# Kernel optimization log

Measured on AMD Instinct MI355X. Metric: run time of the kernel, lower is better.

## Reference

```python
import jax, jax.numpy as jnp
import numpy as np
from jax import lax

EPOCHS = 3
KS = [2, 3, 4, 5]
GRID_D = 5           # sqrt(25): covariance viewed as 5x5 grid of flat indices
M_OUT = 18           # AttentionManifold output SPD size

def _sub_idx(d, k):
    # flat indices of k*k x k*k principal submatrices (stride-1 windows), per SubManifold
    starts = np.arange(0, d - k + 1)
    ir, ic = np.meshgrid(starts, starts, indexing='ij')
    base = (ir * d + ic).reshape(-1)                       # [num_windows]
    a, b = np.meshgrid(np.arange(k), np.arange(k), indexing='ij')
    rel = (a * d + b).reshape(-1)                          # [k*k]
    return base[:, None] + rel[None, :]                    # [num_windows, k*k]

SUB_IDX = [_sub_idx(GRID_D, k) for k in KS]
IN_DIMS = [k * k for k in KS]                              # [4, 9, 16, 25]
IU = np.triu_indices(M_OUT)                                # 171 tangent features
TRI_COEF = np.where(IU[0] == IU[1], 1.0, np.sqrt(2.0)).astype(np.float32)

def _sym_fn(x, fn):
    w, u = jnp.linalg.eigh(x)
    return jnp.einsum('...ik,...k,...jk->...ij', u, fn(w), u)

def spd_log(x, floor=1e-9):
    # matrix log of SPD matrix (== torch.svd-based log for PD input)
    return _sym_fn(x, lambda w: jnp.log(jnp.clip(w, floor)))

def spd_exp(x):
    return _sym_fn(x, jnp.exp)

def spd_rect(x, eps=1e-4):
    # SPDRectified (ReEig): clamp eigenvalues from below
    return _sym_fn(x, lambda w: jnp.clip(w, eps))

def bimap(X, W):
    # SPDTransform: W^T X W, W: [d_in, d_out]
    return jnp.einsum('ia,...ij,jb->...ab', W, X, W)

def diag_jitter(x):
    # deterministic analogue of the random diagonal jitter in SubmanifoldAttention.tensor_log
    n = x.shape[-1]
    return x + jnp.diag((1e-4 / n) * (1.0 + jnp.arange(n, dtype=x.dtype)))

def signal2spd(x):
    # x: [B, C, T] -> trace-normalized covariance [B, C, C]
    x = x - x.mean(-1, keepdims=True)
    cov = jnp.einsum('bct,bdt->bcd', x, x) / (x.shape[-1] - 1)
    tra = jnp.trace(cov, axis1=-2, axis2=-1)[:, None, None]
    cov = cov / tra
    return cov + 1e-5 * jnp.eye(cov.shape[-1], dtype=cov.dtype)

def spd_attention(Q, K, V, jitter):
    # log-maps computed once per element; pairwise log-Euclidean distance via Frobenius identity
    if jitter:
        Q, K, V = diag_jitter(Q), diag_jitter(K), diag_jitter(V)
    logQ, logK = spd_log(Q), spd_log(K)
    qn = jnp.sum(logQ * logQ, (-2, -1))                    # [B, m]
    kn = jnp.sum(logK * logK, (-2, -1))
    cross = jnp.einsum('bixy,bjxy->bij', logK, logQ)
    # E[b,i,j] = ||logQ_j - logK_i||_F^2  (sum of singular values of D D^T)
    E = jnp.maximum(kn[:, :, None] + qn[:, None, :] - 2.0 * cross, 0.0)
    score = 1.0 / (1.0 + jnp.log1p(E))
    P = jnp.swapaxes(jax.nn.softmax(score, axis=-2), -1, -2)  # softmax over i, then permute
    B, m, sz, _ = V.shape
    logV = spd_log(V).reshape(B, m, sz * sz)
    out_log = (P @ logV).reshape(B, m, sz, sz)             # log-Euclidean weighted mean
    out_log = 0.5 * (out_log + jnp.swapaxes(out_log, -1, -2))
    return spd_exp(out_log)

def _bn(y, g, b, m, v):
    inv = g / jnp.sqrt(v + 1e-5)
    return (y - m[None, :, None, None]) * inv[None, :, None, None] + b[None, :, None, None]

def _forward(x, c1w, c1b, bn1g, bn1b, bn1m, bn1v, c2w, c2b, bn2g, bn2b, bn2m, bn2v,
             sq0, sq1, sq2, sq3, sk0, sk1, sk2, sk3, sv0, sv1, sv2, sv3,
             mq, mk, mv, lw, lb):
    dn = ('NCHW', 'OIHW', 'NCHW')
    y = lax.conv_general_dilated(x, c1w, (1, 1), 'VALID', dimension_numbers=dn) + c1b[None, :, None, None]
    y = _bn(y, bn1g, bn1b, bn1m, bn1v)
    y = lax.conv_general_dilated(y, c2w, (1, 1), [(0, 0), (6, 6)], dimension_numbers=dn) + c2b[None, :, None, None]
    y = _bn(y, bn2g, bn2b, bn2m, bn2v)
    sig = y[:, :, 0, :]                                    # squeeze -> [B, 25, T+1]
    T = sig.shape[-1]
    base = T // EPOCHS
    lens = [base + (1 if i < T - base * EPOCHS else 0) for i in range(EPOCHS)]
    covs, off = [], 0
    for Lp in lens:
        covs.append(signal2spd(sig[..., off:off + Lp])); off += Lp
    covs = jnp.stack(covs, axis=1)                         # [B, 3, 25, 25]
    sqs = [sq0, sq1, sq2, sq3]; sks = [sk0, sk1, sk2, sk3]; svs = [sv0, sv1, sv2, sv3]
    branch = []
    for t in range(EPOCHS):
        xb = covs[:, t]                                    # [B, 25, 25]
        Qs, Ks, Vs = [], [], []
        for gi, idx in enumerate(SUB_IDX):
            sub = xb[:, idx[:, :, None], idx[:, None, :]]  # [B, nw, k*k, k*k]
            Qs.append(bimap(sub, sqs[gi]))
            Ks.append(bimap(sub, sks[gi]))
            Vs.append(bimap(sub, svs[gi]))
        att = spd_attention(jnp.concatenate(Qs, 1), jnp.concatenate(Ks, 1),
                            jnp.concatenate(Vs, 1), jitter=True)   # [B, 30, 25, 25]
        branch.append(spd_rect(att[:, -1]))                # keep_only_last
    xm = jnp.stack(branch, axis=1)                         # [B, 3, 25, 25]
    att2 = spd_attention(bimap(xm, mq), bimap(xm, mk), bimap(xm, mv), jitter=False)
    Lg = spd_log(spd_rect(att2))                           # [B, 3, 18, 18]
    feat = (Lg[..., IU[0], IU[1]] * jnp.asarray(TRI_COEF)).reshape(xm.shape[0], -1)
    return feat @ lw.T + lb                                # [B, 4]

def setup_inputs():
    B, T = 256, 1000
    key = jax.random.key(0)
    ks = jax.random.split(key, 40)
    def ortho(k, din, dout):
        a = jax.random.normal(k, (max(din, dout), min(din, dout)), dtype=jnp.float32)
        q, _ = jnp.linalg.qr(a)
        return q if din >= dout else q.T
    inp = {
        'x': jax.random.normal(ks[0], (B, 1, 22, T), dtype=jnp.float32),
        'c1w': 0.1 * jax.random.normal(ks[1], (22, 1, 22, 1), dtype=jnp.float32),
        'c1b': 0.01 * jax.random.normal(ks[2], (22,), dtype=jnp.float32),
        'bn1g': 1.0 + 0.1 * jax.random.normal(ks[3], (22,), dtype=jnp.float32),
        'bn1b': 0.01 * jax.random.normal(ks[4], (22,), dtype=jnp.float32),
        'bn1m': 0.1 * jax.random.normal(ks[5], (22,), dtype=jnp.float32),
        'bn1v': 0.5 + jax.random.uniform(ks[6], (22,), dtype=jnp.float32),
        'c2w': 0.05 * jax.random.normal(ks[7], (25, 22, 1, 12), dtype=jnp.float32),
        'c2b': 0.01 * jax.random.normal(ks[8], (25,), dtype=jnp.float32),
        'bn2g': 1.0 + 0.1 * jax.random.normal(ks[9], (25,), dtype=jnp.float32),
        'bn2b': 0.01 * jax.random.normal(ks[10], (25,), dtype=jnp.float32),
        'bn2m': 0.1 * jax.random.normal(ks[11], (25,), dtype=jnp.float32),
        'bn2v': 0.5 + jax.random.uniform(ks[12], (25,), dtype=jnp.float32),
    }
    for i, din in enumerate(IN_DIMS):
        inp[f'sq{i}'] = ortho(ks[13 + i], din, 4)
        inp[f'sk{i}'] = ortho(ks[17 + i], din, 4)
        inp[f'sv{i}'] = ortho(ks[21 + i], din, 25)
    inp['mq'] = ortho(ks[25], 25, 18)
    inp['mk'] = ortho(ks[26], 25, 18)
    inp['mv'] = ortho(ks[27], 25, 18)
    inp['lw'] = 0.05 * jax.random.normal(ks[28], (4, EPOCHS * len(IU[0])), dtype=jnp.float32)
    inp['lb'] = 0.01 * jax.random.normal(ks[29], (4,), dtype=jnp.float32)
    return inp

def reference(x, c1w, c1b, bn1g, bn1b, bn1m, bn1v, c2w, c2b, bn2g, bn2b, bn2m, bn2v,
              sq0, sq1, sq2, sq3, sk0, sk1, sk2, sk3, sv0, sv1, sv2, sv3,
              mq, mk, mv, lw, lb):
    return _forward(x, c1w, c1b, bn1g, bn1b, bn1m, bn1v, c2w, c2b, bn2g, bn2b, bn2m, bn2v,
                    sq0, sq1, sq2, sq3, sk0, sk1, sk2, sk3, sv0, sv1, sv2, sv3,
                    mq, mk, mv, lw, lb)
```

## Files before the change

kernel.cpp:

```cpp
#include <hip/hip_runtime.h>
#include <hip/hip_bf16.h>
#include <math.h>


__global__ __launch_bounds__(256) void conv1_kernel(
    const float* __restrict__ x, const float* __restrict__ c1w, const float* __restrict__ c1b,
    const float* __restrict__ g, const float* __restrict__ be, const float* __restrict__ mu,
    const float* __restrict__ va, float* __restrict__ ybn1)
{
  __shared__ float w[484];
  __shared__ float scl[22], sft[22];
  int t = threadIdx.x;
  for (int e = t; e < 484; e += 256) w[e] = c1w[e];
  if (t < 22) { float inv = g[t] / sqrtf(va[t] + 1e-5f); scl[t] = inv; sft[t] = be[t] - mu[t]*inv; }
  __syncthreads();
  int gid = blockIdx.x*256 + t;
  int b = gid / 1000, wp = gid % 1000;
  const float* xb = x + (size_t)b*22000 + wp;
  float acc[22];
  #pragma unroll
  for (int o = 0; o < 22; ++o) acc[o] = c1b[o];
  for (int h = 0; h < 22; ++h) {
    float xv = xb[h*1000];
    #pragma unroll
    for (int o = 0; o < 22; ++o) acc[o] += xv * w[o*22 + h];
  }
  float* yb = ybn1 + (size_t)b*22000 + wp;
  #pragma unroll
  for (int o = 0; o < 22; ++o) yb[o*1000] = acc[o]*scl[o] + sft[o];
}

__global__ __launch_bounds__(256) void conv2_kernel(
    const float* __restrict__ ybn1, const float* __restrict__ c2w, const float* __restrict__ c2b,
    const float* __restrict__ g, const float* __restrict__ be, const float* __restrict__ mu,
    const float* __restrict__ va, float* __restrict__ sig)
{
  __shared__ float w[6600];
  __shared__ float scl[25], sft[25];
  int t = threadIdx.x;
  for (int e = t; e < 6600; e += 256) w[e] = c2w[e];
  if (t < 25) { float inv = g[t] / sqrtf(va[t] + 1e-5f); scl[t] = inv; sft[t] = be[t] - mu[t]*inv; }
  __syncthreads();
  int gid = blockIdx.x*256 + t;
  if (gid >= 256*1001) return;
  int b = gid / 1001, wp = gid % 1001;
  const float* yb = ybn1 + (size_t)b*22000;
  float acc[25];
  #pragma unroll
  for (int p = 0; p < 25; ++p) acc[p] = c2b[p];
  for (int c = 0; c < 22; ++c) {
    for (int kw = 0; kw < 12; ++kw) {
      int wi = wp - 6 + kw;
      if (wi < 0 || wi >= 1000) continue;
      float v = yb[c*1000 + wi];
      #pragma unroll
      for (int p = 0; p < 25; ++p) acc[p] += v * w[p*264 + c*12 + kw];
    }
  }
  float* sb = sig + (size_t)b*25025 + wp;
  #pragma unroll
  for (int p = 0; p < 25; ++p) sb[p*1001] = acc[p]*scl[p] + sft[p];
}

__global__ __launch_bounds__(256) void spd_kernel(const float* __restrict__ sig, float* __restrict__ covs)
{
  __shared__ float s[25*334];
  __shared__ float mean[25];
  __shared__ float cv[625];
  __shared__ float tra;
  int bt = blockIdx.x; int b = bt/3, ep = bt%3;
  int off = ep*334;
  int Lp = (ep < 2) ? 334 : 333;
  int t = threadIdx.x;
  const float* sb = sig + (size_t)b*25025;
  for (int e = t; e < 25*Lp; e += 256) { int c = e / Lp, tt = e % Lp; s[c*334 + tt] = sb[c*1001 + off + tt]; }
  __syncthreads();
  if (t < 25) { float m = 0.f; for (int i = 0; i < Lp; ++i) m += s[t*334 + i]; mean[t] = m / (float)Lp; }
  __syncthreads();
  for (int pi = t; pi < 325; pi += 256) {
    int i = 0, rem = pi;
    while (rem >= 25 - i) { rem -= 25 - i; ++i; }
    int j = i + rem;
    float mi = mean[i], mj = mean[j], acc = 0.f;
    for (int k = 0; k < Lp; ++k) acc += (s[i*334 + k] - mi) * (s[j*334 + k] - mj);
    float v = acc / (float)(Lp - 1);
    cv[i*25 + j] = v; cv[j*25 + i] = v;
  }
  __syncthreads();
  if (t == 0) { float tr = 0.f; for (int i = 0; i < 25; ++i) tr += cv[i*26]; tra = tr; }
  __syncthreads();
  float inv = 1.f / tra;
  for (int e = t; e < 625; e += 256) {
    int i = e / 25, j = e % 25;
    covs[(size_t)bt*625 + e] = cv[e]*inv + ((i == j) ? 1e-5f : 0.f);
  }
}

__global__ __launch_bounds__(64) void build_windows_kernel(
    const float* __restrict__ covs,
    const float* __restrict__ sk0, const float* __restrict__ sk1, const float* __restrict__ sk2, const float* __restrict__ sk3,
    const float* __restrict__ sv0, const float* __restrict__ sv1, const float* __restrict__ sv2, const float* __restrict__ sv3,
    const float* __restrict__ sq3,
    float* __restrict__ Vbuf, float* __restrict__ Kbuf, float* __restrict__ Qbuf)
{
  __shared__ float sSub[625], sSv[625], sTmp[625], sSk[100], sTk[100];
  int bw = blockIdx.x;
  int bt = bw / 30, win = bw % 30;
  int t = threadIdx.x;
  int k, r0, c0;
  const float* sv; const float* sk;
  if (win < 16)      { k = 2; r0 = win/4;        c0 = win%4;        sv = sv0; sk = sk0; }
  else if (win < 25) { k = 3; int u = win-16; r0 = u/3; c0 = u%3;   sv = sv1; sk = sk1; }
  else if (win < 29) { k = 4; int u = win-25; r0 = u/2; c0 = u%2;   sv = sv2; sk = sk2; }
  else               { k = 5; r0 = 0;            c0 = 0;            sv = sv3; sk = sk3; }
  int kk = k*k;
  const float* cov = covs + (size_t)bt*625;
  for (int e = t; e < kk*kk; e += 64) {
    int p = e / kk, q = e % kk;
    int ip = (r0 + p/k)*5 + (c0 + p%k);
    int iq = (r0 + q/k)*5 + (c0 + q%k);
    sSub[p*kk + q] = cov[ip*25 + iq];
  }
  for (int e = t; e < kk*25; e += 64) sSv[e] = sv[e];
  for (int e = t; e < kk*4; e += 64)  sSk[e] = sk[e];
  __syncthreads();
  for (int e = t; e < kk*25; e += 64) {
    int i = e / 25, b = e % 25;
    float acc = 0.f;
    for (int j = 0; j < kk; ++j) acc += sSub[i*kk + j] * sSv[j*25 + b];
    sTmp[e] = acc;
  }
  for (int e = t; e < kk*4; e += 64) {
    int i = e / 4, b = e % 4;
    float acc = 0.f;
    for (int j = 0; j < kk; ++j) acc += sSub[i*kk + j] * sSk[j*4 + b];
    sTk[e] = acc;
  }
  __syncthreads();
  float* Vout = Vbuf + (size_t)bw*625;
  for (int e = t; e < 625; e += 64) {
    int a = e / 25, b = e % 25;
    float acc = 0.f;
    for (int i = 0; i < kk; ++i) acc += sSv[i*25 + a] * sTmp[i*25 + b];
    if (a == b) acc += 4e-6f * (float)(1 + a);
    Vout[e] = acc;
  }
  float* Kout = Kbuf + (size_t)bw*16;
  for (int e = t; e < 16; e += 64) {
    int a = e / 4, b = e % 4;
    float acc = 0.f;
    for (int i = 0; i < kk; ++i) acc += sSk[i*4 + a] * sTk[i*4 + b];
    if (a == b) acc += 2.5e-5f * (float)(1 + a);
    Kout[e] = acc;
  }
  if (win == 29) {
    __syncthreads();
    for (int e = t; e < 100; e += 64) {
      int i = e / 4, b = e % 4;
      float acc = 0.f;
      for (int j = 0; j < 25; ++j) acc += sSub[i*25 + j] * sq3[j*4 + b];
      sTk[e] = acc;
    }
    __syncthreads();
    float* Qout = Qbuf + (size_t)bt*16;
    for (int e = t; e < 16; e += 64) {
      int a = e / 4, b = e % 4;
      float acc = 0.f;
      for (int i = 0; i < 25; ++i) acc += sq3[i*4 + a] * sTk[i*4 + b];
      if (a == b) acc += 2.5e-5f * (float)(1 + a);
      Qout[e] = acc;
    }
  }
}

__device__ __forceinline__ float dpp_prev(float v) {
  return __int_as_float(__builtin_amdgcn_update_dpp(0, __float_as_int(v), 0x111, 0xF, 0xF, true));
}
__device__ __forceinline__ float dpp_next(float v) {
  return __int_as_float(__builtin_amdgcn_update_dpp(0, __float_as_int(v), 0x101, 0xF, 0xF, true));
}

template<int NDATA, int MODE, int SHIFT>
__global__ __launch_bounds__(64) void eighbl_kernel(float* __restrict__ mats, float* __restrict__ norms_out)
{
  constexpr int ND    = NDATA;
  constexpr int NPAIR = (NDATA+1)/2;
  constexpr int NPAD  = 2*NPAIR;
  constexpr int NRND  = NPAD-1;
  constexpr int NT    = ND*(ND+1)/2;
  constexpr int STG   = 4*ND*ND;
  constexpr int GNS   = 4*NPAD*ND;
  constexpr int LSZ   = (STG > GNS ? STG : GNS);

  __shared__ float lds[LSZ];
  __shared__ float wv[4*NPAD];

  int t = threadIdx.x;
  int rl = t & 15, mat = t >> 4;
  bool act = rl < NPAIR;
  bool is0 = rl == 0;
  bool isL = rl == NPAIR-1;
  float* M = mats + (size_t)blockIdx.x*4*ND*ND;

  for (int e = t; e < STG; e += 64) lds[e] = M[e];
  __syncthreads();

  const float* st = lds + mat*ND*ND;
  int cA = rl, cB = rl + NPAIR;
  float a[ND], b[ND];
  float na = 0.f, nb = 0.f;
  #pragma unroll
  for (int i = 0; i < ND; ++i) {
    float va = 0.f, vb = 0.f;
    if (act) {
      va = 0.5f*(st[i*ND + cA] + st[cA*ND + i]);
      if (i == cA) va += (float)SHIFT;
      if (cB < ND) {
        vb = 0.5f*(st[i*ND + cB] + st[cB*ND + i]);
        if (i == cB) vb += (float)SHIFT;
      }
    }
    a[i] = va; b[i] = vb;
    na += va*va; nb += vb*vb;
  }

  const float TOL2 = 4e-8f;
  for (int sw = 0; sw < 12; ++sw) {
    int bad = 0;
    #pragma unroll 1
    for (int r = 0; r < NRND; ++r) {
      float d0=0.f,d1=0.f,d2=0.f,d3=0.f,d4=0.f;
      #pragma unroll
      for (int i = 0; i < ND; ++i) {
        float pr = a[i]*b[i];
        if      (i % 5 == 0) d0 += pr;
        else if (i % 5 == 1) d1 += pr;
        else if (i % 5 == 2) d2 += pr;
        else if (i % 5 == 3) d3 += pr;
        else                 d4 += pr;
      }
      float d = ((d0 + d1) + (d2 + d3)) + d4;
      float ad = fabsf(d);
      float dd = (ad > 1e-36f) ? d : 1e-36f;
      float tau = (nb - na) * 0.5f * __builtin_amdgcn_rcpf(dd);
      float mag = __builtin_amdgcn_rcpf(fabsf(tau) + sqrtf(tau*tau + 1.f));
      float tt = copysignf(mag, tau);
      float c = __builtin_amdgcn_rsqf(tt*tt + 1.f);
      float s = tt * c;
      #pragma unroll
      for (int i = 0; i < ND; ++i) {
        float ta = a[i];
        a[i] = c*ta - s*b[i];
        b[i] = s*ta + c*b[i];
      }
      float csd = 2.f*c*s*d;
      float nan_ = c*c*na + s*s*nb - csd;
      float nbn_ = s*s*na + c*c*nb + csd;
      bad |= (act && (d*d > TOL2*na*nb)) ? 1 : 0;
      na = nan_; nb = nbn_;
      #pragma unroll
      for (int i = 0; i < ND; ++i) {
        float tA = dpp_prev(a[i]);
        float tB = dpp_next(b[i]);
        float ao = a[i];
        a[i] = is0 ? tB : tA;
        b[i] = isL ? ao : (is0 ? b[i] : tB);
      }
      {
        float tA = dpp_prev(na);
        float tB = dpp_next(nb);
        float ao = na;
        na = is0 ? tB : tA;
        nb = isL ? ao : (is0 ? nb : tB);
      }
    }
    {
      float n0=0.f,n1=0.f,n2=0.f,n3=0.f,n4=0.f;
      float m0=0.f,m1=0.f,m2=0.f,m3=0.f,m4=0.f;
      #pragma unroll
      for (int i = 0; i < ND; ++i) {
        float pa = a[i]*a[i], pb = b[i]*b[i];
        if      (i % 5 == 0) { n0 += pa; m0 += pb; }
        else if (i % 5 == 1) { n1 += pa; m1 += pb; }
        else if (i % 5 == 2) { n2 += pa; m2 += pb; }
        else if (i % 5 == 3) { n3 += pa; m3 += pb; }
        else                 { n4 += pa; m4 += pb; }
      }
      na = ((n0 + n1) + (n2 + n3)) + n4;
      nb = ((m0 + m1) + (m2 + m3)) + m4;
    }
    if (sw >= 1 && !__any(bad)) break;
  }

  float lamA = sqrtf(na) - (float)SHIFT;
  float lamB = sqrtf(nb) - (float)SHIFT;
  float fA, fB;
  if (MODE == 0)      { fA = logf(fmaxf(lamA, 1e-9f));  fB = logf(fmaxf(lamB, 1e-9f)); }
  else if (MODE == 1) { fA = fmaxf(expf(lamA), 1e-4f);  fB = fmaxf(expf(lamB), 1e-4f); }
  else                { fA = fmaxf(lamA, -9.210340371976182f); fB = fmaxf(lamB, -9.210340371976182f); }
  float wA = (na < 1e-30f) ? 0.f : fA * __builtin_amdgcn_rcpf(na);
  float wB = (nb < 1e-30f) ? 0.f : fB * __builtin_amdgcn_rcpf(nb);

  __syncthreads();
  float* gn = lds + mat*NPAD*ND;
  if (act) {
    #pragma unroll
    for (int i = 0; i < ND; ++i) {
      gn[rl*ND + i] = a[i];
      gn[(rl + NPAIR)*ND + i] = b[i];
    }
    wv[mat*NPAD + rl] = wA;
    wv[mat*NPAD + rl + NPAIR] = wB;
  }
  __syncthreads();

  float wreg[NPAD];
  #pragma unroll
  for (int k = 0; k < NPAD; ++k) wreg[k] = wv[mat*NPAD + k];

  float* Mo = M + mat*ND*ND;
  const float* g = lds + mat*NPAD*ND;
  float nacc = 0.f;
  for (int e = rl; e < NT; e += 16) {
    int i = 0, rem = e;
    while (rem >= ND - i) { rem -= ND - i; ++i; }
    int j = i + rem;
    float acc = 0.f;
    #pragma unroll
    for (int k = 0; k < NPAD; ++k) acc += wreg[k] * g[k*ND + i] * g[k*ND + j];
    Mo[i*ND + j] = acc;
    Mo[j*ND + i] = acc;
    nacc += (i == j) ? acc*acc : 2.f*acc*acc;
  }
  if (norms_out != nullptr) {
    nacc += __shfl_xor(nacc, 8);
    nacc += __shfl_xor(nacc, 4);
    nacc += __shfl_xor(nacc, 2);
    nacc += __shfl_xor(nacc, 1);
    if (rl == 0) norms_out[blockIdx.x*4 + mat] = nacc;
  }
}

template<int P, int Q>
__device__ __forceinline__ void rot4(float a[4][4], float u[4][4])
{
  float apq = a[P][Q];
  if (fabsf(apq) < 1e-36f) return;
  float app = a[P][P], aqq = a[Q][Q];
  float tau = (aqq - app) / (2.f*apq);
  float tt = 1.f / (fabsf(tau) + sqrtf(tau*tau + 1.f));
  if (tau < 0.f) tt = -tt;
  float c = 1.f / sqrtf(tt*tt + 1.f), s = tt*c;
  #pragma unroll
  for (int k = 0; k < 4; ++k) { float akp = a[k][P], akq = a[k][Q]; a[k][P] = c*akp - s*akq; a[k][Q] = s*akp + c*akq; }
  #pragma unroll
  for (int k = 0; k < 4; ++k) { float apk = a[P][k], aqk = a[Q][k]; a[P][k] = c*apk - s*aqk; a[Q][k] = s*apk + c*aqk; }
  #pragma unroll
  for (int k = 0; k < 4; ++k) { float ukp = u[k][P], ukq = u[k][Q]; u[k][P] = c*ukp - s*ukq; u[k][Q] = s*ukp + c*ukq; }
}

__global__ __launch_bounds__(256) void eigh4_kernel(float* __restrict__ kmats, float* __restrict__ qmats,
                                                    float* __restrict__ norms)
{
  int idx = blockIdx.x*256 + threadIdx.x;
  if (idx >= 23808) return;
  float* M = (idx < 23040) ? (kmats + (size_t)idx*16) : (qmats + (size_t)(idx - 23040)*16);
  float a[4][4], u[4][4];
  #pragma unroll
  for (int i = 0; i < 4; ++i)
    #pragma unroll
    for (int j = 0; j < 4; ++j) { a[i][j] = 0.5f*(M[i*4+j] + M[j*4+i]); u[i][j] = (i == j) ? 1.f : 0.f; }
  #pragma unroll 1
  for (int sw = 0; sw < 8; ++sw) {
    rot4<0,1>(a,u); rot4<0,2>(a,u); rot4<0,3>(a,u);
    rot4<1,2>(a,u); rot4<1,3>(a,u); rot4<2,3>(a,u);
  }
  float f[4];
  #pragma unroll
  for (int i = 0; i < 4; ++i) f[i] = logf(fmaxf(a[i][i], 1e-9f));
  float nrm = 0.f;
  #pragma unroll
  for (int i = 0; i < 4; ++i)
    #pragma unroll
    for (int j = 0; j < 4; ++j) {
      float acc = 0.f;
      #pragma unroll
      for (int k = 0; k < 4; ++k) acc += u[i][k]*f[k]*u[j][k];
      M[i*4+j] = acc; nrm += acc*acc;
    }
  norms[idx] = nrm;
}

__global__ __launch_bounds__(64) void att1_kernel(
    const float* __restrict__ logK, const float* __restrict__ logQ,
    const float* __restrict__ kn, const float* __restrict__ qn,
    const float* __restrict__ logV, float* __restrict__ outlog1)
{
  __shared__ float lq[16];
  __shared__ float sscore[30];
  __shared__ float sp[30];
  int bt = blockIdx.x, t = threadIdx.x;
  if (t < 16) lq[t] = logQ[(size_t)bt*16 + t];
  __syncthreads();
  if (t < 30) {
    const float* lk = logK + ((size_t)bt*30 + t)*16;
    float cr = 0.f;
    #pragma unroll
    for (int e = 0; e < 16; ++e) cr += lk[e]*lq[e];
    float E = fmaxf(kn[bt*30 + t] + qn[bt] - 2.f*cr, 0.f);
    sscore[t] = 1.f/(1.f + log1pf(E));
  }
  __syncthreads();
  float mx = -1e30f;
  for (int i = 0; i < 30; ++i) mx = fmaxf(mx, sscore[i]);
  float sm = 0.f;
  for (int i = 0; i < 30; ++i) sm += expf(sscore[i] - mx);
  if (t < 30) sp[t] = expf(sscore[t] - mx)/sm;
  __syncthreads();
  const float* lv = logV + (size_t)bt*30*625;
  float* outp = outlog1 + (size_t)bt*625;
  for (int e = t; e < 625; e += 64) {
    float acc = 0.f;
    for (int i = 0; i < 30; ++i) acc += sp[i]*lv[(size_t)i*625 + e];
    outp[e] = acc;
  }
}

__global__ __launch_bounds__(64) void qkv2_kernel(
    const float* __restrict__ xm, const float* __restrict__ mq, const float* __restrict__ mk,
    const float* __restrict__ mv, float* __restrict__ q2, float* __restrict__ k2, float* __restrict__ v2)
{
  __shared__ float sx[625], sw[450], stmp[450];
  int bt = blockIdx.x, t = threadIdx.x;
  for (int e = t; e < 625; e += 64) sx[e] = xm[(size_t)bt*625 + e];
  for (int wi = 0; wi < 3; ++wi) {
    const float* W = (wi == 0) ? mq : (wi == 1) ? mk : mv;
    float* O = ((wi == 0) ? q2 : (wi == 1) ? k2 : v2) + (size_t)bt*324;
    for (int e = t; e < 450; e += 64) sw[e] = W[e];
    __syncthreads();
    for (int e = t; e < 450; e += 64) {
      int i = e / 18, b = e % 18;
      float acc = 0.f;
      for (int j = 0; j < 25; ++j) acc += sx[i*25 + j]*sw[j*18 + b];
      stmp[e] = acc;
    }
    __syncthreads();
    for (int e = t; e < 324; e += 64) {
      int a = e / 18, b = e % 18;
      float acc = 0.f;
      for (int i = 0; i < 25; ++i) acc += sw[i*18 + a]*stmp[i*18 + b];
      O[e] = acc;
    }
    __syncthreads();
  }
}

__global__ __launch_bounds__(64) void att2_kernel(
    const float* __restrict__ logQ2, const float* __restrict__ logK2, const float* __restrict__ logV2,
    const float* __restrict__ norms, float* __restrict__ outlog2)
{
  __shared__ float S[3][3];
  __shared__ float PT[3][3];
  int b = blockIdx.x, t = threadIdx.x;
  if (t < 9) {
    int i = t / 3, j = t % 3;
    const float* lk = logK2 + ((size_t)b*3 + i)*324;
    const float* lq = logQ2 + ((size_t)b*3 + j)*324;
    float cr = 0.f;
    for (int e = 0; e < 324; ++e) cr += lk[e]*lq[e];
    float E = fmaxf(norms[768 + b*3 + i] + norms[b*3 + j] - 2.f*cr, 0.f);
    S[i][j] = 1.f/(1.f + log1pf(E));
  }
  __syncthreads();
  if (t < 3) {
    float m = fmaxf(S[0][t], fmaxf(S[1][t], S[2][t]));
    float e0 = expf(S[0][t]-m), e1 = expf(S[1][t]-m), e2 = expf(S[2][t]-m);
    float ssum = e0 + e1 + e2;
    PT[t][0] = e0/ssum; PT[t][1] = e1/ssum; PT[t][2] = e2/ssum;
  }
  __syncthreads();
  for (int e = t; e < 324; e += 64) {
    float l0 = logV2[((size_t)b*3 + 0)*324 + e];
    float l1 = logV2[((size_t)b*3 + 1)*324 + e];
    float l2 = logV2[((size_t)b*3 + 2)*324 + e];
    #pragma unroll
    for (int j = 0; j < 3; ++j)
      outlog2[((size_t)b*3 + j)*324 + e] = PT[j][0]*l0 + PT[j][1]*l1 + PT[j][2]*l2;
  }
}

__global__ __launch_bounds__(64) void feat_kernel(
    const float* __restrict__ Lg, const float* __restrict__ lw, const float* __restrict__ lb,
    float* __restrict__ outp)
{
  __shared__ int tri_i[171], tri_j[171];
  int b = blockIdx.x, t = threadIdx.x;
  if (t == 0) { int f = 0; for (int i = 0; i < 18; ++i) for (int j = i; j < 18; ++j) { tri_i[f] = i; tri_j[f] = j; ++f; } }
  __syncthreads();
  float a0 = 0.f, a1 = 0.f, a2 = 0.f, a3 = 0.f;
  const float SQ2 = 1.41421356237309515f;
  for (int f = t; f < 513; f += 64) {
    int tt = f / 171, r = f % 171;
    int i = tri_i[r], j = tri_j[r];
    float coef = (i == j) ? 1.f : SQ2;
    float v = Lg[((size_t)b*3 + tt)*324 + i*18 + j] * coef;
    a0 += v*lw[0*513 + f]; a1 += v*lw[1*513 + f]; a2 += v*lw[2*513 + f]; a3 += v*lw[3*513 + f];
  }
  #pragma unroll
  for (int off = 32; off > 0; off >>= 1) {
    a0 += __shfl_down(a0, off); a1 += __shfl_down(a1, off);
    a2 += __shfl_down(a2, off); a3 += __shfl_down(a3, off);
  }
  if (t == 0) {
    outp[b*4 + 0] = a0 + lb[0]; outp[b*4 + 1] = a1 + lb[1];
    outp[b*4 + 2] = a2 + lb[2]; outp[b*4 + 3] = a3 + lb[3];
  }
}

extern "C" void kernel_launch(void* const* d_in, const int* in_sizes, int n_in,
                              void* d_out, int out_size, void* d_ws, size_t ws_size,
                              hipStream_t stream)
{
  const float* x    = (const float*)d_in[0];
  const float* c1w  = (const float*)d_in[1];
  const float* c1b  = (const float*)d_in[2];
  const float* bn1g = (const float*)d_in[3];
  const float* bn1b = (const float*)d_in[4];
  const float* bn1m = (const float*)d_in[5];
  const float* bn1v = (const float*)d_in[6];
  const float* c2w  = (const float*)d_in[7];
  const float* c2b  = (const float*)d_in[8];
  const float* bn2g = (const float*)d_in[9];
  const float* bn2b = (const float*)d_in[10];
  const float* bn2m = (const float*)d_in[11];
  const float* bn2v = (const float*)d_in[12];
  const float* sk0  = (const float*)d_in[14];
  const float* sv0  = (const float*)d_in[15];
  const float* sk1  = (const float*)d_in[17];
  const float* sv1  = (const float*)d_in[18];
  const float* sk2  = (const float*)d_in[20];
  const float* sv2  = (const float*)d_in[21];
  const float* sq3  = (const float*)d_in[22];
  const float* sk3  = (const float*)d_in[23];
  const float* sv3  = (const float*)d_in[24];
  const float* mq   = (const float*)d_in[25];
  const float* mk   = (const float*)d_in[26];
  const float* mv   = (const float*)d_in[27];
  const float* lw   = (const float*)d_in[28];
  const float* lb   = (const float*)d_in[29];
  float* outp = (float*)d_out;

  float* ws = (float*)d_ws;
  float* covs = ws;
  float* ybn1 = ws + 480000;
  float* sig  = ws + 6112000;
  float* Vbuf = ws + 480000;
  float* Kbuf = ws + 14880000;
  float* Qbuf = ws + 15248640;
  float* knb  = ws + 15260928;
  float* ol1  = ws + 15284736;
  float* qkv2 = ws + 15764736;
  float* nrm2 = ws + 16511232;
  float* ol2  = ws + 16513536;

  conv1_kernel<<<1000, 256, 0, stream>>>(x, c1w, c1b, bn1g, bn1b, bn1m, bn1v, ybn1);
  conv2_kernel<<<1001, 256, 0, stream>>>(ybn1, c2w, c2b, bn2g, bn2b, bn2m, bn2v, sig);
  spd_kernel<<<768, 256, 0, stream>>>(sig, covs);
  build_windows_kernel<<<23040, 64, 0, stream>>>(covs, sk0, sk1, sk2, sk3, sv0, sv1, sv2, sv3, sq3,
                                                 Vbuf, Kbuf, Qbuf);
  eighbl_kernel<25,0,0><<<5760, 64, 0, stream>>>(Vbuf, nullptr);
  eigh4_kernel<<<93, 256, 0, stream>>>(Kbuf, Qbuf, knb);
  att1_kernel<<<768, 64, 0, stream>>>(Kbuf, Qbuf, knb, knb + 23040, Vbuf, ol1);
  eighbl_kernel<25,1,16><<<192, 64, 0, stream>>>(ol1, nullptr);
  qkv2_kernel<<<768, 64, 0, stream>>>(ol1, mq, mk, mv, qkv2, qkv2 + 248832, qkv2 + 497664);
  eighbl_kernel<18,0,0><<<576, 64, 0, stream>>>(qkv2, nrm2);
  att2_kernel<<<256, 64, 0, stream>>>(qkv2, qkv2 + 248832, qkv2 + 497664, nrm2, ol2);
  eighbl_kernel<18,2,16><<<192, 64, 0, stream>>>(ol2, nullptr);
  feat_kernel<<<256, 64, 0, stream>>>(ol2, lw, lb, outp);
}
```

Measured before the change: 1.372 ms.

## Replace round-robin one-sided Jacobi with odd-even ordering in eigensolver

Switches the one-sided Jacobi eigensolver from a round-robin (Brent-Luk) pairing with DPP shifts of every column to an odd-even transposition ordering. Each lane holds adjacent columns, and each round does an intra-lane rotation followed by a cross-lane rotation through neighbour DPP moves. The aim is fewer register shuffles per rotation. The sweep cap drops from 12 to 9 and several multiply-adds become explicit fmaf. Odd-even ordering may need more sweeps to converge, and the lower cap risks accuracy on hard matrices.

```diff
diff --git a/kernel.cpp b/kernel.cpp
--- a/kernel.cpp
+++ b/kernel.cpp
@@ -181,33 +181,33 @@
 }
 
 template<int NDATA, int MODE, int SHIFT>
-__global__ __launch_bounds__(64) void eighbl_kernel(float* __restrict__ mats, float* __restrict__ norms_out)
-{
-  constexpr int ND    = NDATA;
-  constexpr int NPAIR = (NDATA+1)/2;
-  constexpr int NPAD  = 2*NPAIR;
-  constexpr int NRND  = NPAD-1;
-  constexpr int NT    = ND*(ND+1)/2;
-  constexpr int STG   = 4*ND*ND;
-  constexpr int GNS   = 4*NPAD*ND;
-  constexpr int LSZ   = (STG > GNS ? STG : GNS);
+__global__ __launch_bounds__(64) void eighoe_kernel(float* __restrict__ mats, float* __restrict__ norms_out)
+{
+  constexpr int ND   = NDATA;
+  constexpr int NPOS = (ND + 1) & ~1;
+  constexpr int NH   = NPOS/2;
+  constexpr int NT   = ND*(ND+1)/2;
+  constexpr int STG  = 4*ND*ND;
+  constexpr int GNS  = 4*NPOS*ND;
+  constexpr int LSZ  = (STG > GNS ? STG : GNS);
 
   __shared__ float lds[LSZ];
-  __shared__ float wv[4*NPAD];
+  __shared__ float wv[4*NPOS];
 
   int t = threadIdx.x;
   int rl = t & 15, mat = t >> 4;
-  bool act = rl < NPAIR;
-  bool is0 = rl == 0;
-  bool isL = rl == NPAIR-1;
+  bool act   = rl < NH;
+  bool isL   = rl == NH-1;
+  bool actB  = act && !isL;
+  bool recvA = (rl >= 1) && (rl < NH);
   float* M = mats + (size_t)blockIdx.x*4*ND*ND;
 
   for (int e = t; e < STG; e += 64) lds[e] = M[e];
   __syncthreads();
 
   const float* st = lds + mat*ND*ND;
-  int cA = rl, cB = rl + NPAIR;
-  float a[ND], b[ND];
+  int cA = 2*rl, cB = 2*rl + 1;
+  float a[ND], b[ND], ta[ND];
   float na = 0.f, nb = 0.f;
   #pragma unroll
   for (int i = 0; i < ND; ++i) {
@@ -221,57 +221,83 @@
       }
     }
     a[i] = va; b[i] = vb;
-    na += va*va; nb += vb*vb;
+    na = fmaf(va, va, na); nb = fmaf(vb, vb, nb);
   }
 
   const float TOL2 = 4e-8f;
-  for (int sw = 0; sw < 12; ++sw) {
+  for (int sw = 0; sw < 9; ++sw) {
     int bad = 0;
     #pragma unroll 1
-    for (int r = 0; r < NRND; ++r) {
-      float d0=0.f,d1=0.f,d2=0.f,d3=0.f,d4=0.f;
-      #pragma unroll
-      for (int i = 0; i < ND; ++i) {
-        float pr = a[i]*b[i];
-        if      (i % 5 == 0) d0 += pr;
-        else if (i % 5 == 1) d1 += pr;
-        else if (i % 5 == 2) d2 += pr;
-        else if (i % 5 == 3) d3 += pr;
-        else                 d4 += pr;
-      }
-      float d = ((d0 + d1) + (d2 + d3)) + d4;
-      float ad = fabsf(d);
-      float dd = (ad > 1e-36f) ? d : 1e-36f;
-      float tau = (nb - na) * 0.5f * __builtin_amdgcn_rcpf(dd);
-      float mag = __builtin_amdgcn_rcpf(fabsf(tau) + sqrtf(tau*tau + 1.f));
-      float tt = copysignf(mag, tau);
-      float c = __builtin_amdgcn_rsqf(tt*tt + 1.f);
-      float s = tt * c;
-      #pragma unroll
-      for (int i = 0; i < ND; ++i) {
-        float ta = a[i];
-        a[i] = c*ta - s*b[i];
-        b[i] = s*ta + c*b[i];
-      }
-      float csd = 2.f*c*s*d;
-      float nan_ = c*c*na + s*s*nb - csd;
-      float nbn_ = s*s*na + c*c*nb + csd;
-      bad |= (act && (d*d > TOL2*na*nb)) ? 1 : 0;
-      na = nan_; nb = nbn_;
-      #pragma unroll
-      for (int i = 0; i < ND; ++i) {
-        float tA = dpp_prev(a[i]);
-        float tB = dpp_next(b[i]);
-        float ao = a[i];
-        a[i] = is0 ? tB : tA;
-        b[i] = isL ? ao : (is0 ? b[i] : tB);
+    for (int rr = 0; rr < NH; ++rr) {
+      {
+        float d0=0.f,d1=0.f,d2=0.f,d3=0.f,d4=0.f;
+        #pragma unroll
+        for (int i = 0; i < ND; ++i) {
+          if      (i % 5 == 0) d0 = fmaf(a[i], b[i], d0);
+          else if (i % 5 == 1) d1 = fmaf(a[i], b[i], d1);
+          else if (i % 5 == 2) d2 = fmaf(a[i], b[i], d2);
+          else if (i % 5 == 3) d3 = fmaf(a[i], b[i], d3);
+          else                 d4 = fmaf(a[i], b[i], d4);
+        }
+        float d = ((d0 + d1) + (d2 + d3)) + d4;
+        float ad = fabsf(d);
+        float dd = (ad > 1e-36f) ? d : 1e-36f;
+        float tau = (nb - na) * 0.5f * __builtin_amdgcn_rcpf(dd);
+        float mag = __builtin_amdgcn_rcpf(fabsf(tau) + sqrtf(fmaf(tau, tau, 1.f)));
+        float tt = copysignf(mag, tau);
+        float c = __builtin_amdgcn_rsqf(fmaf(tt, tt, 1.f));
+        float s = tt * c;
+        #pragma unroll
+        for (int i = 0; i < ND; ++i) {
+          float av = a[i], bv = b[i];
+          a[i] = fmaf(s, av,  c*bv);
+          b[i] = fmaf(c, av, -(s*bv));
+        }
+        bad |= (act && (d*d > TOL2*na*nb)) ? 1 : 0;
+        float csd = 2.f*c*s*d;
+        float c2 = c*c, s2 = s*s;
+        float nA = s2*na + c2*nb + csd;
+        float nB = c2*na + s2*nb - csd;
+        na = nA; nb = nB;
       }
       {
-        float tA = dpp_prev(na);
-        float tB = dpp_next(nb);
-        float ao = na;
-        na = is0 ? tB : tA;
-        nb = isL ? ao : (is0 ? nb : tB);
+        #pragma unroll
+        for (int i = 0; i < ND; ++i) ta[i] = dpp_next(a[i]);
+        float n_ta = dpp_next(na);
+        float d0=0.f,d1=0.f,d2=0.f,d3=0.f,d4=0.f;
+        #pragma unroll
+        for (int i = 0; i < ND; ++i) {
+          if      (i % 5 == 0) d0 = fmaf(b[i], ta[i], d0);
+          else if (i % 5 == 1) d1 = fmaf(b[i], ta[i], d1);
+          else if (i % 5 == 2) d2 = fmaf(b[i], ta[i], d2);
+          else if (i % 5 == 3) d3 = fmaf(b[i], ta[i], d3);
+          else                 d4 = fmaf(b[i], ta[i], d4);
+        }
+        float d = ((d0 + d1) + (d2 + d3)) + d4;
+        float ad = fabsf(d);
+        float dd = (ad > 1e-36f) ? d : 1e-36f;
+        float tau = (n_ta - nb) * 0.5f * __builtin_amdgcn_rcpf(dd);
+        float mag = __builtin_amdgcn_rcpf(fabsf(tau) + sqrtf(fmaf(tau, tau, 1.f)));
+        float tt = copysignf(mag, tau);
+        float c = __builtin_amdgcn_rsqf(fmaf(tt, tt, 1.f));
+        float s = tt * c;
+        #pragma unroll
+        for (int i = 0; i < ND; ++i) {
+          float bv = b[i], tv = ta[i];
+          float qv = fmaf(s, bv,  c*tv);
+          float pv = fmaf(c, bv, -(s*tv));
+          float sh = dpp_prev(pv);
+          b[i] = actB  ? qv : b[i];
+          a[i] = recvA ? sh : a[i];
+        }
+        bad |= (actB && (d*d > TOL2*nb*n_ta)) ? 1 : 0;
+        float csd = 2.f*c*s*d;
+        float c2 = c*c, s2 = s*s;
+        float nq  = s2*nb + c2*n_ta + csd;
+        float npv = c2*nb + s2*n_ta - csd;
+        float shn = dpp_prev(npv);
+        nb = actB  ? nq  : nb;
+        na = recvA ? shn : na;
       }
     }
     {
@@ -279,12 +305,11 @@
       float m0=0.f,m1=0.f,m2=0.f,m3=0.f,m4=0.f;
       #pragma unroll
       for (int i = 0; i < ND; ++i) {
-        float pa = a[i]*a[i], pb = b[i]*b[i];
-        if      (i % 5 == 0) { n0 += pa; m0 += pb; }
-        else if (i % 5 == 1) { n1 += pa; m1 += pb; }
-        else if (i % 5 == 2) { n2 += pa; m2 += pb; }
-        else if (i % 5 == 3) { n3 += pa; m3 += pb; }
-        else                 { n4 += pa; m4 += pb; }
+        if      (i % 5 == 0) { n0 = fmaf(a[i],a[i],n0); m0 = fmaf(b[i],b[i],m0); }
+        else if (i % 5 == 1) { n1 = fmaf(a[i],a[i],n1); m1 = fmaf(b[i],b[i],m1); }
+        else if (i % 5 == 2) { n2 = fmaf(a[i],a[i],n2); m2 = fmaf(b[i],b[i],m2); }
+        else if (i % 5 == 3) { n3 = fmaf(a[i],a[i],n3); m3 = fmaf(b[i],b[i],m3); }
+        else                 { n4 = fmaf(a[i],a[i],n4); m4 = fmaf(b[i],b[i],m4); }
       }
       na = ((n0 + n1) + (n2 + n3)) + n4;
       nb = ((m0 + m1) + (m2 + m3)) + m4;
@@ -302,24 +327,24 @@
   float wB = (nb < 1e-30f) ? 0.f : fB * __builtin_amdgcn_rcpf(nb);
 
   __syncthreads();
-  float* gn = lds + mat*NPAD*ND;
+  float* gn = lds + mat*NPOS*ND;
   if (act) {
     #pragma unroll
     for (int i = 0; i < ND; ++i) {
       gn[rl*ND + i] = a[i];
-      gn[(rl + NPAIR)*ND + i] = b[i];
-    }
-    wv[mat*NPAD + rl] = wA;
-    wv[mat*NPAD + rl + NPAIR] = wB;
-  }
-  __syncthreads();
-
-  float wreg[NPAD];
-  #pragma unroll
-  for (int k = 0; k < NPAD; ++k) wreg[k] = wv[mat*NPAD + k];
+      gn[(rl + NH)*ND + i] = b[i];
+    }
+    wv[mat*NPOS + rl] = wA;
+    wv[mat*NPOS + rl + NH] = wB;
+  }
+  __syncthreads();
+
+  float wreg[NPOS];
+  #pragma unroll
+  for (int k = 0; k < NPOS; ++k) wreg[k] = wv[mat*NPOS + k];
 
   float* Mo = M + mat*ND*ND;
-  const float* g = lds + mat*NPAD*ND;
+  const float* g = lds + mat*NPOS*ND;
   float nacc = 0.f;
   for (int e = rl; e < NT; e += 16) {
     int i = 0, rem = e;
@@ -327,7 +352,10 @@
     int j = i + rem;
     float acc = 0.f;
     #pragma unroll
-    for (int k = 0; k < NPAD; ++k) acc += wreg[k] * g[k*ND + i] * g[k*ND + j];
+    for (int k = 0; k < NPOS; ++k) {
+      float wg = wreg[k] * g[k*ND + i];
+      acc = fmaf(wg, g[k*ND + j], acc);
+    }
     Mo[i*ND + j] = acc;
     Mo[j*ND + i] = acc;
     nacc += (i == j) ? acc*acc : 2.f*acc*acc;
@@ -568,13 +596,13 @@
   spd_kernel<<<768, 256, 0, stream>>>(sig, covs);
   build_windows_kernel<<<23040, 64, 0, stream>>>(covs, sk0, sk1, sk2, sk3, sv0, sv1, sv2, sv3, sq3,
                                                  Vbuf, Kbuf, Qbuf);
-  eighbl_kernel<25,0,0><<<5760, 64, 0, stream>>>(Vbuf, nullptr);
+  eighoe_kernel<25,0,0><<<5760, 64, 0, stream>>>(Vbuf, nullptr);
   eigh4_kernel<<<93, 256, 0, stream>>>(Kbuf, Qbuf, knb);
   att1_kernel<<<768, 64, 0, stream>>>(Kbuf, Qbuf, knb, knb + 23040, Vbuf, ol1);
-  eighbl_kernel<25,1,16><<<192, 64, 0, stream>>>(ol1, nullptr);
+  eighoe_kernel<25,1,16><<<192, 64, 0, stream>>>(ol1, nullptr);
   qkv2_kernel<<<768, 64, 0, stream>>>(ol1, mq, mk, mv, qkv2, qkv2 + 248832, qkv2 + 497664);
-  eighbl_kernel<18,0,0><<<576, 64, 0, stream>>>(qkv2, nrm2);
+  eighoe_kernel<18,0,0><<<576, 64, 0, stream>>>(qkv2, nrm2);
   att2_kernel<<<256, 64, 0, stream>>>(qkv2, qkv2 + 248832, qkv2 + 497664, nrm2, ol2);
-  eighbl_kernel<18,2,16><<<192, 64, 0, stream>>>(ol2, nullptr);
+  eighoe_kernel<18,2,16><<<192, 64, 0, stream>>>(ol2, nullptr);
   feat_kernel<<<256, 64, 0, stream>>>(ol2, lw, lb, outp);
 }
```

After: 1.201 ms. 1.14x faster.
